# Kernel tuning notes

Hardware: AMD Instinct MI355X
Metric: run time of the kernel (lower is better)

## Reference

```python
import jax, jax.numpy as jnp
import numpy as np

ALPHA = -300.0        # softmax sharpness (negative -> weight nearest bin)
IS_QUAN_ON = 1.0      # 1.0 = fully quantized output
B, L, K = 4096, 512, 32


def setup_inputs() -> dict:
    key = jax.random.key(0)
    kx, kb = jax.random.split(key)
    x = jax.random.normal(kx, (B, L, 1), dtype=jnp.float32)
    # codebook bins: sorted scalar centers (kmeans-like init)
    bins = jnp.sort(jax.random.normal(kb, (K,), dtype=jnp.float32))
    return {"x": x, "bins": bins}


def reference(x, bins):
    # x: (B, L, 1), bins: (K,)
    dist = jnp.abs(x - bins.reshape(1, 1, -1))          # (B, L, K)
    soft_assignment = jax.nn.softmax(ALPHA * dist, axis=-1)  # (B, L, K)
    # soft-quantized code: weighted sum of bin values -> (B, L, 1)
    bit_code = jnp.einsum('blk,k->bl', soft_assignment, bins)[..., None]
    bit_code = (1.0 - IS_QUAN_ON) * x + IS_QUAN_ON * bit_code
    return soft_assignment, bit_code
```

## Files before the change

kernel.cpp:

```cpp
#include <hip/hip_runtime.h>


#define SSQ_SCALE (-432.80854f)
#define SSQ_UNROLL 4

typedef float f32x4 __attribute__((ext_vector_type(4)));

template <int CTRL>
__device__ __forceinline__ float dpp_f(float v) {
    int i = __builtin_bit_cast(int, v);
    i = __builtin_amdgcn_update_dpp(i, i, CTRL, 0xf, 0xf, true);
    return __builtin_bit_cast(float, i);
}
#define DPP_XOR1  0xB1
#define DPP_XOR2  0x4E
#define DPP_HMIRR 0x141

__device__ __forceinline__ float red8_max(float v) {
    v = fmaxf(v, dpp_f<DPP_XOR1>(v));
    v = fmaxf(v, dpp_f<DPP_XOR2>(v));
    v = fmaxf(v, dpp_f<DPP_HMIRR>(v));
    return v;
}
__device__ __forceinline__ float red8_sum(float v) {
    v += dpp_f<DPP_XOR1>(v);
    v += dpp_f<DPP_XOR2>(v);
    v += dpp_f<DPP_HMIRR>(v);
    return v;
}

__global__ __launch_bounds__(256) void ssq_kernel(
    const float* __restrict__ x,
    const float* __restrict__ bins,
    float* __restrict__ soft,
    float* __restrict__ code,
    int total_vec)
{
    const int sub = threadIdx.x & 7;
    const f32x4 b4 = reinterpret_cast<const f32x4*>(bins)[sub];
    f32x4* __restrict__ soft4 = reinterpret_cast<f32x4*>(soft);

    const int base = blockIdx.x * (256 * SSQ_UNROLL) + threadIdx.x;

    int   f[SSQ_UNROLL];
    bool  act[SSQ_UNROLL];
    float xv[SSQ_UNROLL];

    #pragma unroll
    for (int u = 0; u < SSQ_UNROLL; ++u) {
        f[u] = base + u * 256;
        act[u] = f[u] < total_vec;
        xv[u] = act[u] ? x[f[u] >> 3] : 0.0f;
    }

    #pragma unroll
    for (int u = 0; u < SSQ_UNROLL; ++u) {
        if (!act[u]) continue;
        const float xu = xv[u];

        float s0 = SSQ_SCALE * fabsf(xu - b4.x);
        float s1 = SSQ_SCALE * fabsf(xu - b4.y);
        float s2 = SSQ_SCALE * fabsf(xu - b4.z);
        float s3 = SSQ_SCALE * fabsf(xu - b4.w);

        float m = red8_max(fmaxf(fmaxf(s0, s1), fmaxf(s2, s3)));

        float e0 = exp2f(s0 - m);
        float e1 = exp2f(s1 - m);
        float e2 = exp2f(s2 - m);
        float e3 = exp2f(s3 - m);

        float sum = red8_sum((e0 + e1) + (e2 + e3));
        float num = red8_sum((e0 * b4.x + e1 * b4.y) + (e2 * b4.z + e3 * b4.w));

        const float inv = __builtin_amdgcn_rcpf(sum);
        f32x4 w;
        w.x = e0 * inv; w.y = e1 * inv; w.z = e2 * inv; w.w = e3 * inv;
        soft4[f[u]] = w;

        if (sub == 0) code[f[u] >> 3] = num * inv;
    }
}

extern "C" void kernel_launch(void* const* d_in, const int* in_sizes, int n_in,
                              void* d_out, int out_size, void* d_ws, size_t ws_size,
                              hipStream_t stream) {
    const float* x    = (const float*)d_in[0];
    const float* bins = (const float*)d_in[1];
    const int n = in_sizes[0];

    float* soft = (float*)d_out;
    float* code = soft + (size_t)n * 32;

    const int total_vec = n * 8;
    const int block = 256;
    const int grid  = (total_vec + block * SSQ_UNROLL - 1) / (block * SSQ_UNROLL);
    ssq_kernel<<<grid, block, 0, stream>>>(x, bins, soft, code, total_vec);
}
```

Baseline: 61.12 us.

## Switch to fixed-grid persistent blocks with XCD-aware chunking and prefetched x

Replaces the one-shot unrolled grid with a fixed 2048-block grid. Each block loops over a contiguous chunk of iterations, and the x load for the next iteration is prefetched one step ahead. Block indices are remapped so that consecutive blocks on the same XCD get adjacent chunks. The max-of-scaled-logits reduction becomes a min-distance reduction with fused FMA for exp arguments, which trims a few ALU ops. This risks less memory-level parallelism per thread than the four independent unrolled items, and the grid may be imbalanced when the size does not divide evenly.

```diff
diff --git a/kernel.cpp b/kernel.cpp
--- a/kernel.cpp
+++ b/kernel.cpp
@@ -2,7 +2,7 @@
 
 
 #define SSQ_SCALE (-432.80854f)
-#define SSQ_UNROLL 4
+#define SSQ_BLOCKS 2048
 
 typedef float f32x4 __attribute__((ext_vector_type(4)));
 
@@ -16,10 +16,10 @@
 #define DPP_XOR2  0x4E
 #define DPP_HMIRR 0x141
 
-__device__ __forceinline__ float red8_max(float v) {
-    v = fmaxf(v, dpp_f<DPP_XOR1>(v));
-    v = fmaxf(v, dpp_f<DPP_XOR2>(v));
-    v = fmaxf(v, dpp_f<DPP_HMIRR>(v));
+__device__ __forceinline__ float red8_min(float v) {
+    v = fminf(v, dpp_f<DPP_XOR1>(v));
+    v = fminf(v, dpp_f<DPP_XOR2>(v));
+    v = fminf(v, dpp_f<DPP_HMIRR>(v));
     return v;
 }
 __device__ __forceinline__ float red8_sum(float v) {
@@ -34,51 +34,50 @@
     const float* __restrict__ bins,
     float* __restrict__ soft,
     float* __restrict__ code,
-    int total_vec)
+    int total_vec,
+    int iters)
 {
     const int sub = threadIdx.x & 7;
     const f32x4 b4 = reinterpret_cast<const f32x4*>(bins)[sub];
     f32x4* __restrict__ soft4 = reinterpret_cast<f32x4*>(soft);
 
-    const int base = blockIdx.x * (256 * SSQ_UNROLL) + threadIdx.x;
+    const int chunk = (blockIdx.x & 7) * (SSQ_BLOCKS / 8) + (blockIdx.x >> 3);
+    const int base  = chunk * (iters * 256) + threadIdx.x;
 
-    int   f[SSQ_UNROLL];
-    bool  act[SSQ_UNROLL];
-    float xv[SSQ_UNROLL];
+    float xv = (base < total_vec) ? x[base >> 3] : 0.0f;
 
-    #pragma unroll
-    for (int u = 0; u < SSQ_UNROLL; ++u) {
-        f[u] = base + u * 256;
-        act[u] = f[u] < total_vec;
-        xv[u] = act[u] ? x[f[u] >> 3] : 0.0f;
-    }
+    for (int it = 0; it < iters; ++it) {
+        const int f = base + it * 256;
+        if (f >= total_vec) break;
 
-    #pragma unroll
-    for (int u = 0; u < SSQ_UNROLL; ++u) {
-        if (!act[u]) continue;
-        const float xu = xv[u];
+        const int fn = f + 256;
+        float xn = 0.0f;
+        if (it + 1 < iters && fn < total_vec) xn = x[fn >> 3];
 
-        float s0 = SSQ_SCALE * fabsf(xu - b4.x);
-        float s1 = SSQ_SCALE * fabsf(xu - b4.y);
-        float s2 = SSQ_SCALE * fabsf(xu - b4.z);
-        float s3 = SSQ_SCALE * fabsf(xu - b4.w);
+        const float d0 = fabsf(xv - b4.x);
+        const float d1 = fabsf(xv - b4.y);
+        const float d2 = fabsf(xv - b4.z);
+        const float d3 = fabsf(xv - b4.w);
+        const float dmin = red8_min(fminf(fminf(d0, d1), fminf(d2, d3)));
 
-        float m = red8_max(fmaxf(fmaxf(s0, s1), fmaxf(s2, s3)));
+        const float moff = -SSQ_SCALE * dmin;
+        const float e0 = exp2f(fmaf(SSQ_SCALE, d0, moff));
+        const float e1 = exp2f(fmaf(SSQ_SCALE, d1, moff));
+        const float e2 = exp2f(fmaf(SSQ_SCALE, d2, moff));
+        const float e3 = exp2f(fmaf(SSQ_SCALE, d3, moff));
 
-        float e0 = exp2f(s0 - m);
-        float e1 = exp2f(s1 - m);
-        float e2 = exp2f(s2 - m);
-        float e3 = exp2f(s3 - m);
-
-        float sum = red8_sum((e0 + e1) + (e2 + e3));
-        float num = red8_sum((e0 * b4.x + e1 * b4.y) + (e2 * b4.z + e3 * b4.w));
+        const float sum = red8_sum((e0 + e1) + (e2 + e3));
+        const float num = red8_sum((e0 * b4.x + e1 * b4.y) +
+                                   (e2 * b4.z + e3 * b4.w));
 
         const float inv = __builtin_amdgcn_rcpf(sum);
         f32x4 w;
         w.x = e0 * inv; w.y = e1 * inv; w.z = e2 * inv; w.w = e3 * inv;
-        soft4[f[u]] = w;
+        soft4[f] = w;
 
-        if (sub == 0) code[f[u] >> 3] = num * inv;
+        if (sub == 0) code[f >> 3] = num * inv;
+
+        xv = xn;
     }
 }
 
@@ -93,7 +92,9 @@
     float* code = soft + (size_t)n * 32;
 
     const int total_vec = n * 8;
-    const int block = 256;
-    const int grid  = (total_vec + block * SSQ_UNROLL - 1) / (block * SSQ_UNROLL);
-    ssq_kernel<<<grid, block, 0, stream>>>(x, bins, soft, code, total_vec);
+    const int per_blk_unit = 256;
+    const int iters = (total_vec + SSQ_BLOCKS * per_blk_unit - 1) /
+                      (SSQ_BLOCKS * per_blk_unit);
+    ssq_kernel<<<SSQ_BLOCKS, 256, 0, stream>>>(x, bins, soft, code,
+                                               total_vec, iters);
 }
```

After: 83.48 us. +36.6%, slower.
